# Kernel optimization log

Hardware: AMD Instinct MI355X
Metric: run time of the kernel (lower is better)

Reference implementation:

```python
import jax, jax.numpy as jnp
import numpy as np

CROSS_PRUNE = 0.1  # matches init_kwargs cross_prune

N, T, D, M = 100000, 64, 128, 8


def setup_inputs() -> dict:
    key = jax.random.key(0)
    k1, k2, k3, k4 = jax.random.split(key, 4)
    x = jax.random.normal(k1, (N, D), dtype=jnp.float32)          # graph node features
    mats = jax.random.normal(k2, (M, T, D), dtype=jnp.float32) * 0.1  # cross mats (kaiming-ish scale)
    head_w = jax.random.normal(k3, (M,), dtype=jnp.float32) * 0.3     # task_head.weight [1, M] squeezed
    head_b = jax.random.normal(k4, (), dtype=jnp.float32) * 0.1       # task_head.bias
    return {"x": x, "mats": mats, "head_w": head_w, "head_b": head_b}


def reference(x, mats, head_w, head_b):
    # Original: for each mat m, cross_dot_m = mat_m @ x.T  -> M mats of [T, N];
    # then per-(i,j): task_head([cross_dot_m[i,j] for m]) = sum_m w_m * cross_dot_m[i,j] + b.
    # Linearity lets us contract the head weight into the mats first (identical math,
    # avoids materializing the [M, T, N] stack the torch code builds element-by-element).
    w_mat = jnp.einsum('m,mtd->td', head_w, mats)          # [T, D]
    cross_dot = jnp.einsum('td,nd->tn', w_mat, x) + head_b  # [T, N]
    cross_sim = jax.nn.sigmoid(cross_dot)
    # prune: entries below threshold -> 0 (dense adjacency; edge_index extraction in the
    # original is just nonzero() over this matrix, which has data-dependent shape)
    cross_adj = jnp.where(cross_sim < CROSS_PRUNE, jnp.zeros_like(cross_sim), cross_sim)
    return cross_adj
```

## Files before the change

### kernel.cpp

```cpp
#include <hip/hip_runtime.h>
#include <hip/hip_bf16.h>

#define N_NODES 100000
#define T_DIM 64
#define D_DIM 128
#define M_MATS 8
#define CROSS_PRUNE 0.1f
#define WPLANE (T_DIM * D_DIM)

typedef __attribute__((ext_vector_type(8))) short bf16x8;
typedef __attribute__((ext_vector_type(4))) float f32x4;
typedef __attribute__((ext_vector_type(8))) unsigned short ushort8;

__device__ __forceinline__ void split3(float v, unsigned short& h,
                                       unsigned short& m, unsigned short& l) {
    __hip_bfloat16 bh = __float2bfloat16(v);
    float fh = __bfloat162float(bh);
    float r1 = v - fh;
    __hip_bfloat16 bm = __float2bfloat16(r1);
    float fm = __bfloat162float(bm);
    float r2 = r1 - fm;
    __hip_bfloat16 bl = __float2bfloat16(r2);
    h = __builtin_bit_cast(unsigned short, bh);
    m = __builtin_bit_cast(unsigned short, bm);
    l = __builtin_bit_cast(unsigned short, bl);
}

__global__ __launch_bounds__(256) void wsplit_kernel(const float* __restrict__ mats,
                                                     const float* __restrict__ head_w,
                                                     unsigned short* __restrict__ wh,
                                                     unsigned short* __restrict__ wm,
                                                     unsigned short* __restrict__ wl) {
    int i = blockIdx.x * 256 + threadIdx.x;
    if (i < WPLANE) {
        float acc = 0.f;
#pragma unroll
        for (int m = 0; m < M_MATS; ++m)
            acc += head_w[m] * mats[m * WPLANE + i];
        unsigned short h, mm, l;
        split3(acc, h, mm, l);
        wh[i] = h; wm[i] = mm; wl[i] = l;
    }
}

__global__ __launch_bounds__(256, 3) void cross_kernel(const float* __restrict__ x,
                                                       const unsigned short* __restrict__ wh,
                                                       const unsigned short* __restrict__ wm,
                                                       const unsigned short* __restrict__ wl,
                                                       const float* __restrict__ head_b_p,
                                                       float* __restrict__ out) {
    __shared__ unsigned short xh[WPLANE];
    __shared__ unsigned short xm[WPLANE];
    __shared__ unsigned short xl[WPLANE];

    const int tid = threadIdx.x;
    const int n0 = blockIdx.x * 64;
    const int lane = tid & 63;
    const int tg = tid >> 6;
    const int r = lane & 15;
    const int q = lane >> 4;

    const int srow = tid >> 2;
    const int c4 = tid & 3;
    const int gn_s = n0 + srow;
    const float* xrow = x + (size_t)gn_s * D_DIM + c4 * 32;

    float4 p[8];
#pragma unroll
    for (int j = 0; j < 8; ++j) {
        p[j] = make_float4(0.f, 0.f, 0.f, 0.f);
        if (gn_s < N_NODES)
            p[j] = *reinterpret_cast<const float4*>(xrow + j * 4);
    }

    bf16x8 ah[4], am[4], al[4];
#pragma unroll
    for (int k4 = 0; k4 < 4; ++k4) {
        int eo = (tg * 16 + r) * D_DIM + k4 * 32 + q * 8;
        ah[k4] = *reinterpret_cast<const bf16x8*>(wh + eo);
        am[k4] = *reinterpret_cast<const bf16x8*>(wm + eo);
        al[k4] = *reinterpret_cast<const bf16x8*>(wl + eo);
    }

    {
        float fv[32];
#pragma unroll
        for (int j = 0; j < 8; ++j) {
            fv[j * 4 + 0] = p[j].x; fv[j * 4 + 1] = p[j].y;
            fv[j * 4 + 2] = p[j].z; fv[j * 4 + 3] = p[j].w;
        }
#pragma unroll
        for (int u = 0; u < 4; ++u) {
            ushort8 H, M, L;
#pragma unroll
            for (int e = 0; e < 8; ++e) {
                unsigned short h_, m_, l_;
                split3(fv[u * 8 + e], h_, m_, l_);
                H[e] = h_; M[e] = m_; L[e] = l_;
            }
            int unit = srow * 16 + c4 * 4 + u;
            int byte = (unit << 4) ^ ((srow & 7) << 4);
            *reinterpret_cast<ushort8*>(reinterpret_cast<char*>(xh) + byte) = H;
            *reinterpret_cast<ushort8*>(reinterpret_cast<char*>(xm) + byte) = M;
            *reinterpret_cast<ushort8*>(reinterpret_cast<char*>(xl) + byte) = L;
        }
    }
    __syncthreads();

    f32x4 acc[4];
#pragma unroll
    for (int nt = 0; nt < 4; ++nt) acc[nt] = (f32x4){0.f, 0.f, 0.f, 0.f};

#pragma unroll
    for (int k4 = 0; k4 < 4; ++k4) {
        bf16x8 bh[4], bm[4], bl[4];
#pragma unroll
        for (int nt = 0; nt < 4; ++nt) {
            int eo = (nt * 16 + r) * D_DIM + k4 * 32 + q * 8;
            int byte = (eo << 1) ^ ((r & 7) << 4);
            bh[nt] = *reinterpret_cast<const bf16x8*>(reinterpret_cast<const char*>(xh) + byte);
            bm[nt] = *reinterpret_cast<const bf16x8*>(reinterpret_cast<const char*>(xm) + byte);
            bl[nt] = *reinterpret_cast<const bf16x8*>(reinterpret_cast<const char*>(xl) + byte);
        }
#pragma unroll
        for (int nt = 0; nt < 4; ++nt)
            acc[nt] = __builtin_amdgcn_mfma_f32_16x16x32_bf16(ah[k4], bh[nt], acc[nt], 0, 0, 0);
#pragma unroll
        for (int nt = 0; nt < 4; ++nt)
            acc[nt] = __builtin_amdgcn_mfma_f32_16x16x32_bf16(ah[k4], bm[nt], acc[nt], 0, 0, 0);
#pragma unroll
        for (int nt = 0; nt < 4; ++nt)
            acc[nt] = __builtin_amdgcn_mfma_f32_16x16x32_bf16(am[k4], bh[nt], acc[nt], 0, 0, 0);
#pragma unroll
        for (int nt = 0; nt < 4; ++nt)
            acc[nt] = __builtin_amdgcn_mfma_f32_16x16x32_bf16(ah[k4], bl[nt], acc[nt], 0, 0, 0);
#pragma unroll
        for (int nt = 0; nt < 4; ++nt)
            acc[nt] = __builtin_amdgcn_mfma_f32_16x16x32_bf16(al[k4], bh[nt], acc[nt], 0, 0, 0);
#pragma unroll
        for (int nt = 0; nt < 4; ++nt)
            acc[nt] = __builtin_amdgcn_mfma_f32_16x16x32_bf16(am[k4], bm[nt], acc[nt], 0, 0, 0);
    }

    const float hb = head_b_p[0];
#pragma unroll
    for (int nt = 0; nt < 4; ++nt) {
        int n = n0 + nt * 16 + r;
        if (n < N_NODES) {
#pragma unroll
            for (int i = 0; i < 4; ++i) {
                int t = tg * 16 + q * 4 + i;
                float v = acc[nt][i] + hb;
                float s = 1.0f / (1.0f + __expf(-v));
                if (s < CROSS_PRUNE) s = 0.0f;
                out[(size_t)t * N_NODES + n] = s;
            }
        }
    }
}

extern "C" void kernel_launch(void* const* d_in, const int* in_sizes, int n_in,
                              void* d_out, int out_size, void* d_ws, size_t ws_size,
                              hipStream_t stream) {
    const float* x      = (const float*)d_in[0];
    const float* mats   = (const float*)d_in[1];
    const float* head_w = (const float*)d_in[2];
    const float* head_b = (const float*)d_in[3];
    float* out = (float*)d_out;

    unsigned short* wh = (unsigned short*)d_ws;
    unsigned short* wm = wh + WPLANE;
    unsigned short* wl = wm + WPLANE;

    hipLaunchKernelGGL(wsplit_kernel, dim3((WPLANE + 255) / 256), dim3(256), 0, stream,
                       mats, head_w, wh, wm, wl);

    int nblk = (N_NODES + 63) / 64;
    hipLaunchKernelGGL(cross_kernel, dim3(nblk), dim3(256), 0, stream,
                       x, wh, wm, wl, head_b, out);
}
```

Before: 35.16 us.

## Load x directly into MFMA fragments per wave, dropping shared-memory staging

```diff
diff --git a/kernel.cpp b/kernel.cpp
--- a/kernel.cpp
+++ b/kernel.cpp
@@ -10,7 +10,6 @@
 
 typedef __attribute__((ext_vector_type(8))) short bf16x8;
 typedef __attribute__((ext_vector_type(4))) float f32x4;
-typedef __attribute__((ext_vector_type(8))) unsigned short ushort8;
 
 __device__ __forceinline__ void split3(float v, unsigned short& h,
                                        unsigned short& m, unsigned short& l) {
@@ -24,6 +23,17 @@
     h = __builtin_bit_cast(unsigned short, bh);
     m = __builtin_bit_cast(unsigned short, bm);
     l = __builtin_bit_cast(unsigned short, bl);
+}
+
+__device__ __forceinline__ void split8(float4 v0, float4 v1,
+                                       bf16x8& H, bf16x8& M, bf16x8& L) {
+    float fv[8] = {v0.x, v0.y, v0.z, v0.w, v1.x, v1.y, v1.z, v1.w};
+#pragma unroll
+    for (int e = 0; e < 8; ++e) {
+        unsigned short h_, m_, l_;
+        split3(fv[e], h_, m_, l_);
+        H[e] = (short)h_; M[e] = (short)m_; L[e] = (short)l_;
+    }
 }
 
 __global__ __launch_bounds__(256) void wsplit_kernel(const float* __restrict__ mats,
@@ -43,35 +53,18 @@
     }
 }
 
-__global__ __launch_bounds__(256, 3) void cross_kernel(const float* __restrict__ x,
+__global__ __launch_bounds__(256, 4) void cross_kernel(const float* __restrict__ x,
                                                        const unsigned short* __restrict__ wh,
                                                        const unsigned short* __restrict__ wm,
                                                        const unsigned short* __restrict__ wl,
                                                        const float* __restrict__ head_b_p,
                                                        float* __restrict__ out) {
-    __shared__ unsigned short xh[WPLANE];
-    __shared__ unsigned short xm[WPLANE];
-    __shared__ unsigned short xl[WPLANE];
-
     const int tid = threadIdx.x;
-    const int n0 = blockIdx.x * 64;
     const int lane = tid & 63;
     const int tg = tid >> 6;
     const int r = lane & 15;
     const int q = lane >> 4;
-
-    const int srow = tid >> 2;
-    const int c4 = tid & 3;
-    const int gn_s = n0 + srow;
-    const float* xrow = x + (size_t)gn_s * D_DIM + c4 * 32;
-
-    float4 p[8];
-#pragma unroll
-    for (int j = 0; j < 8; ++j) {
-        p[j] = make_float4(0.f, 0.f, 0.f, 0.f);
-        if (gn_s < N_NODES)
-            p[j] = *reinterpret_cast<const float4*>(xrow + j * 4);
-    }
+    const int n0 = blockIdx.x * 64;
 
     bf16x8 ah[4], am[4], al[4];
 #pragma unroll
@@ -82,64 +75,47 @@
         al[k4] = *reinterpret_cast<const bf16x8*>(wl + eo);
     }
 
-    {
-        float fv[32];
-#pragma unroll
-        for (int j = 0; j < 8; ++j) {
-            fv[j * 4 + 0] = p[j].x; fv[j * 4 + 1] = p[j].y;
-            fv[j * 4 + 2] = p[j].z; fv[j * 4 + 3] = p[j].w;
-        }
-#pragma unroll
-        for (int u = 0; u < 4; ++u) {
-            ushort8 H, M, L;
-#pragma unroll
-            for (int e = 0; e < 8; ++e) {
-                unsigned short h_, m_, l_;
-                split3(fv[u * 8 + e], h_, m_, l_);
-                H[e] = h_; M[e] = m_; L[e] = l_;
-            }
-            int unit = srow * 16 + c4 * 4 + u;
-            int byte = (unit << 4) ^ ((srow & 7) << 4);
-            *reinterpret_cast<ushort8*>(reinterpret_cast<char*>(xh) + byte) = H;
-            *reinterpret_cast<ushort8*>(reinterpret_cast<char*>(xm) + byte) = M;
-            *reinterpret_cast<ushort8*>(reinterpret_cast<char*>(xl) + byte) = L;
-        }
-    }
-    __syncthreads();
-
     f32x4 acc[4];
 #pragma unroll
     for (int nt = 0; nt < 4; ++nt) acc[nt] = (f32x4){0.f, 0.f, 0.f, 0.f};
 
+    const float4 z4 = make_float4(0.f, 0.f, 0.f, 0.f);
+
 #pragma unroll
     for (int k4 = 0; k4 < 4; ++k4) {
-        bf16x8 bh[4], bm[4], bl[4];
+        const int dofs = k4 * 32 + q * 8;
 #pragma unroll
-        for (int nt = 0; nt < 4; ++nt) {
-            int eo = (nt * 16 + r) * D_DIM + k4 * 32 + q * 8;
-            int byte = (eo << 1) ^ ((r & 7) << 4);
-            bh[nt] = *reinterpret_cast<const bf16x8*>(reinterpret_cast<const char*>(xh) + byte);
-            bm[nt] = *reinterpret_cast<const bf16x8*>(reinterpret_cast<const char*>(xm) + byte);
-            bl[nt] = *reinterpret_cast<const bf16x8*>(reinterpret_cast<const char*>(xl) + byte);
+        for (int np = 0; np < 4; np += 2) {
+            const int na = n0 + np * 16 + r;
+            const int nb = na + 16;
+            float4 a0 = z4, a1 = z4, b0 = z4, b1 = z4;
+            if (na < N_NODES) {
+                const float* pa = x + (size_t)na * D_DIM + dofs;
+                a0 = *reinterpret_cast<const float4*>(pa);
+                a1 = *reinterpret_cast<const float4*>(pa + 4);
+            }
+            if (nb < N_NODES) {
+                const float* pb = x + (size_t)nb * D_DIM + dofs;
+                b0 = *reinterpret_cast<const float4*>(pb);
+                b1 = *reinterpret_cast<const float4*>(pb + 4);
+            }
+            bf16x8 bhA, bmA, blA, bhB, bmB, blB;
+            split8(a0, a1, bhA, bmA, blA);
+            split8(b0, b1, bhB, bmB, blB);
+
+            acc[np]     = __builtin_amdgcn_mfma_f32_16x16x32_bf16(ah[k4], bhA, acc[np], 0, 0, 0);
+            acc[np + 1] = __builtin_amdgcn_mfma_f32_16x16x32_bf16(ah[k4], bhB, acc[np + 1], 0, 0, 0);
+            acc[np]     = __builtin_amdgcn_mfma_f32_16x16x32_bf16(ah[k4], bmA, acc[np], 0, 0, 0);
+            acc[np + 1] = __builtin_amdgcn_mfma_f32_16x16x32_bf16(ah[k4], bmB, acc[np + 1], 0, 0, 0);
+            acc[np]     = __builtin_amdgcn_mfma_f32_16x16x32_bf16(am[k4], bhA, acc[np], 0, 0, 0);
+            acc[np + 1] = __builtin_amdgcn_mfma_f32_16x16x32_bf16(am[k4], bhB, acc[np + 1], 0, 0, 0);
+            acc[np]     = __builtin_amdgcn_mfma_f32_16x16x32_bf16(ah[k4], blA, acc[np], 0, 0, 0);
+            acc[np + 1] = __builtin_amdgcn_mfma_f32_16x16x32_bf16(ah[k4], blB, acc[np + 1], 0, 0, 0);
+            acc[np]     = __builtin_amdgcn_mfma_f32_16x16x32_bf16(al[k4], bhA, acc[np], 0, 0, 0);
+            acc[np + 1] = __builtin_amdgcn_mfma_f32_16x16x32_bf16(al[k4], bhB, acc[np + 1], 0, 0, 0);
+            acc[np]     = __builtin_amdgcn_mfma_f32_16x16x32_bf16(am[k4], bmA, acc[np], 0, 0, 0);
+            acc[np + 1] = __builtin_amdgcn_mfma_f32_16x16x32_bf16(am[k4], bmB, acc[np + 1], 0, 0, 0);
         }
-#pragma unroll
-        for (int nt = 0; nt < 4; ++nt)
-            acc[nt] = __builtin_amdgcn_mfma_f32_16x16x32_bf16(ah[k4], bh[nt], acc[nt], 0, 0, 0);
-#pragma unroll
-        for (int nt = 0; nt < 4; ++nt)
-            acc[nt] = __builtin_amdgcn_mfma_f32_16x16x32_bf16(ah[k4], bm[nt], acc[nt], 0, 0, 0);
-#pragma unroll
-        for (int nt = 0; nt < 4; ++nt)
-            acc[nt] = __builtin_amdgcn_mfma_f32_16x16x32_bf16(am[k4], bh[nt], acc[nt], 0, 0, 0);
-#pragma unroll
-        for (int nt = 0; nt < 4; ++nt)
-            acc[nt] = __builtin_amdgcn_mfma_f32_16x16x32_bf16(ah[k4], bl[nt], acc[nt], 0, 0, 0);
-#pragma unroll
-        for (int nt = 0; nt < 4; ++nt)
-            acc[nt] = __builtin_amdgcn_mfma_f32_16x16x32_bf16(al[k4], bh[nt], acc[nt], 0, 0, 0);
-#pragma unroll
-        for (int nt = 0; nt < 4; ++nt)
-            acc[nt] = __builtin_amdgcn_mfma_f32_16x16x32_bf16(am[k4], bm[nt], acc[nt], 0, 0, 0);
     }
 
     const float hb = head_b_p[0];
```

Measured after the change: 48.23 us. 1.37x slower.
